# Kernel tuning notes

Measured on AMD Instinct MI355X. Metric: run time of the kernel, lower is better.

The kernel has to match this reference:

```python
import jax, jax.numpy as jnp
import numpy as np

DISTANCE_THRESHOLD = 100.0  # squared-distance threshold (cdist**2 <= thresh)
NO_CODE_ID = -1


def setup_inputs() -> dict:
    key = jax.random.key(0)
    kx, kc = jax.random.split(key)
    x = jax.random.normal(kx, (2, 1024, 64), dtype=jnp.float32)      # [b, s, d] query tokens
    codes = jax.random.normal(kc, (50000, 64), dtype=jnp.float32)    # [n, d] active code bank
    return {"x": x, "codes": codes}


def reference(x, codes):
    # squared euclidean distances, matching torch.cdist(x, codes) ** 2
    x2 = jnp.sum(x * x, axis=-1, keepdims=True)            # [b, s, 1]
    c2 = jnp.sum(codes * codes, axis=-1)                   # [n]
    cross = jnp.einsum('bsd,nd->bsn', x, codes)            # [b, s, n]
    d2 = jnp.maximum(x2 + c2 - 2.0 * cross, 0.0)           # clamp tiny negatives, cdist >= 0

    within = jnp.any(d2 <= DISTANCE_THRESHOLD, axis=-1)    # [b, s]
    nn_ids = jnp.argmin(d2, axis=-1)                       # [b, s]
    return jnp.where(within, nn_ids, NO_CODE_ID)
```

## Files before the change

### kernel.cpp

```cpp
#include <hip/hip_runtime.h>

#define NTOK   2048
#define DIM    64
#define NCODES 50000
#define THRESH 100.0f
#define BIG    3.0e38f
#define MARGIN 4.0f
#define NBLK   391
#define BM32   1564
#define BM32P  1568
#define NCG    64

typedef __attribute__((ext_vector_type(8)))  __bf16 bf16x8;
typedef __attribute__((ext_vector_type(16))) float  float16;

__device__ __forceinline__ unsigned short f2bf(float f) {
    union { float f; unsigned int u; } v; v.f = f;
    unsigned int r = v.u + 0x7FFF + ((v.u >> 16) & 1);
    return (unsigned short)(r >> 16);
}
__device__ __forceinline__ unsigned int pack2(float a, float b) {
    return (unsigned int)f2bf(a) | ((unsigned int)f2bf(b) << 16);
}

__global__ __launch_bounds__(256)
void nn_prep_kernel(const float* __restrict__ x, const float* __restrict__ codes,
                    unsigned short* __restrict__ cbf, unsigned short* __restrict__ xbf,
                    float* __restrict__ c2, float* __restrict__ x2,
                    float* __restrict__ bm32) {
    int g = blockIdx.x * 256 + threadIdx.x;
    if (g < NTOK * 4) {
        int t = g >> 2;
        bm32[(size_t)t * BM32P + BM32 + (g & 3)] = BIG;
    }
    int row = g >> 2;
    int seg = g & 3;
    const float* src;
    unsigned short* dst;
    float* nrm;
    if (row < NCODES) {
        src = codes + (size_t)row * DIM + seg * 16;
        dst = cbf + (size_t)row * DIM + seg * 16;
        nrm = (seg == 0) ? (c2 + row) : nullptr;
    } else if (row < NCODES + NTOK) {
        int r = row - NCODES;
        src = x + (size_t)r * DIM + seg * 16;
        dst = xbf + (size_t)r * DIM + seg * 16;
        nrm = (seg == 0) ? (x2 + r) : nullptr;
    } else {
        return;
    }
    float4 v0 = ((const float4*)src)[0];
    float4 v1 = ((const float4*)src)[1];
    float4 v2 = ((const float4*)src)[2];
    float4 v3 = ((const float4*)src)[3];
    float s = 0.f;
    s = fmaf(v0.x, v0.x, s); s = fmaf(v0.y, v0.y, s);
    s = fmaf(v0.z, v0.z, s); s = fmaf(v0.w, v0.w, s);
    s = fmaf(v1.x, v1.x, s); s = fmaf(v1.y, v1.y, s);
    s = fmaf(v1.z, v1.z, s); s = fmaf(v1.w, v1.w, s);
    s = fmaf(v2.x, v2.x, s); s = fmaf(v2.y, v2.y, s);
    s = fmaf(v2.z, v2.z, s); s = fmaf(v2.w, v2.w, s);
    s = fmaf(v3.x, v3.x, s); s = fmaf(v3.y, v3.y, s);
    s = fmaf(v3.z, v3.z, s); s = fmaf(v3.w, v3.w, s);
    uint4 lo, hi;
    lo.x = pack2(v0.x, v0.y); lo.y = pack2(v0.z, v0.w);
    lo.z = pack2(v1.x, v1.y); lo.w = pack2(v1.z, v1.w);
    hi.x = pack2(v2.x, v2.y); hi.y = pack2(v2.z, v2.w);
    hi.z = pack2(v3.x, v3.y); hi.w = pack2(v3.z, v3.w);
    *(uint4*)dst = lo;
    *(uint4*)(dst + 8) = hi;
    s += __shfl_xor(s, 1);
    s += __shfl_xor(s, 2);
    if (nrm) *nrm = s;
}

__global__ __launch_bounds__(256, 2)
void nn_stageA_kernel(const unsigned short* __restrict__ xbf,
                      const unsigned short* __restrict__ cbf,
                      const float* __restrict__ c2g,
                      float* __restrict__ bm32) {
    __shared__ __bf16 cs[128 * 72];
    __shared__ float  c2s[128];

    const int tid  = threadIdx.x;
    const int w    = tid >> 6;
    const int lane = tid & 63;
    const int l31  = lane & 31;
    const int h    = lane >> 5;
    const int gi   = blockIdx.x;
    const int g0   = 6 * gi + min(gi, 7);
    const int nb   = (gi < 7) ? 7 : 6;
    const int t0   = blockIdx.y * 256;

    bf16x8 bfr[4][2];
#pragma unroll
    for (int s = 0; s < 4; ++s)
#pragma unroll
        for (int nj = 0; nj < 2; ++nj)
            bfr[s][nj] = *(const bf16x8*)&xbf[
                (size_t)(t0 + w * 64 + nj * 32 + l31) * DIM + s * 16 + h * 8];

    uint4 pr[4];
    float prc;
    auto prefetch = [&](int blk) {
        int n0 = blk * 128;
#pragma unroll
        for (int it = 0; it < 4; ++it) {
            int g = it * 256 + tid;
            int row = g >> 3, seg = g & 7;
            int n = n0 + row;
            pr[it] = (n < NCODES) ? *(const uint4*)(cbf + (size_t)n * DIM + seg * 8)
                                  : make_uint4(0, 0, 0, 0);
        }
        if (tid < 128) {
            int n = n0 + tid;
            prc = (n < NCODES) ? c2g[n] : BIG;
        }
    };
    prefetch(g0);

    for (int t = 0; t < nb; ++t) {
        const int blk = g0 + t;
        __syncthreads();

#pragma unroll
        for (int it = 0; it < 4; ++it) {
            int g = it * 256 + tid;
            int row = g >> 3, seg = g & 7;
            *(uint4*)&cs[row * 72 + seg * 8] = pr[it];
        }
        if (tid < 128) c2s[tid] = prc;
        if (t + 1 < nb) prefetch(blk + 1);
        __syncthreads();

        float16 acc[4][2];
#pragma unroll
        for (int mi = 0; mi < 4; ++mi) {
#pragma unroll
            for (int g2 = 0; g2 < 4; ++g2) {
                float4 c4 = *(float4*)&c2s[mi * 32 + g2 * 8 + 4 * h];
#pragma unroll
                for (int i = 0; i < 4; ++i) {
                    float iv = -0.5f * ((float*)&c4)[i];
                    acc[mi][0][g2 * 4 + i] = iv;
                    acc[mi][1][g2 * 4 + i] = iv;
                }
            }
        }

#pragma unroll
        for (int s = 0; s < 4; ++s) {
            bf16x8 a[4];
#pragma unroll
            for (int mi = 0; mi < 4; ++mi)
                a[mi] = *(bf16x8*)&cs[(mi * 32 + l31) * 72 + s * 16 + h * 8];
#pragma unroll
            for (int mi = 0; mi < 4; ++mi)
#pragma unroll
                for (int nj = 0; nj < 2; ++nj)
                    acc[mi][nj] = __builtin_amdgcn_mfma_f32_32x32x16_bf16(
                        a[mi], bfr[s][nj], acc[mi][nj], 0, 0, 0);
        }

#pragma unroll
        for (int nj = 0; nj < 2; ++nj) {
            float4 o;
#pragma unroll
            for (int mi = 0; mi < 4; ++mi) {
                float m = acc[mi][nj][0];
#pragma unroll
                for (int r = 1; r < 16; ++r) m = fmaxf(m, acc[mi][nj][r]);
                m = fmaxf(m, __shfl_xor(m, 32));
                ((float*)&o)[mi] = -2.0f * m;
            }
            if (lane < 32) {
                int token = t0 + w * 64 + nj * 32 + lane;
                *(float4*)&bm32[(size_t)token * BM32P + blk * 4] = o;
            }
        }
    }
}

__global__ __launch_bounds__(256)
void nn_finalize_kernel(const float* __restrict__ x,
                        const float* __restrict__ codes,
                        const float* __restrict__ c2,
                        const float* __restrict__ x2,
                        const float* __restrict__ bm32,
                        int* __restrict__ out) {
    __shared__ float redf[8];
    __shared__ int   redi[4];
    __shared__ int   queue[BM32P];
    __shared__ int   qcount;
    __shared__ float gshare;

    const int tid  = threadIdx.x;
    const int w    = tid >> 6;
    const int lane = tid & 63;
    const int t    = blockIdx.x;
    const float* bm = bm32 + (size_t)t * BM32P;

    if (tid == 0) qcount = 0;

    float v[7];
    float g = BIG;
#pragma unroll
    for (int k = 0; k < 7; ++k) {
        int b = tid + k * 256;
        v[k] = (b < BM32P) ? bm[b] : BIG;
        g = fminf(g, v[k]);
    }
#pragma unroll
    for (int m = 1; m < 64; m <<= 1) g = fminf(g, __shfl_xor(g, m));
    if (lane == 0) redf[w] = g;
    __syncthreads();
    if (tid == 0)
        gshare = fminf(fminf(redf[0], redf[1]), fminf(redf[2], redf[3])) + MARGIN;
    __syncthreads();
    const float th = gshare;

#pragma unroll
    for (int k = 0; k < 7; ++k) {
        int b = tid + k * 256;
        if (b < BM32P && v[k] <= th) {
            int slot = atomicAdd(&qcount, 1);
            queue[slot] = b;
        }
    }
    __syncthreads();
    const int nq = qcount;

    const int half = lane & 1;
    float4 xh[8];
#pragma unroll
    for (int q = 0; q < 8; ++q)
        xh[q] = *(const float4*)(x + (size_t)t * DIM + half * 32 + q * 4);
    const float x2v = x2[t];

    float bv = BIG;
    int   bi = 0x7fffffff;
    for (int e = w; e < nq; e += 4) {
        int blk = queue[e];
        int n = blk * 32 + (lane >> 1);
        if (n < NCODES) {
            const float4* cp = (const float4*)(codes + (size_t)n * DIM + half * 32);
            float d = 0.f;
#pragma unroll
            for (int q = 0; q < 8; ++q) {
                float4 c4 = cp[q];
                d = fmaf(xh[q].x, c4.x, d);
                d = fmaf(xh[q].y, c4.y, d);
                d = fmaf(xh[q].z, c4.z, d);
                d = fmaf(xh[q].w, c4.w, d);
            }
            d += __shfl_xor(d, 1);
            float d2 = fmaxf(fmaf(-2.f, d, x2v + c2[n]), 0.f);
            if (d2 < bv || (d2 == bv && n < bi)) { bv = d2; bi = n; }
        }
    }
#pragma unroll
    for (int m = 1; m < 64; m <<= 1) {
        float vv = __shfl_xor(bv, m);
        int   ii = __shfl_xor(bi, m);
        if (vv < bv || (vv == bv && ii < bi)) { bv = vv; bi = ii; }
    }
    if (lane == 0) { redf[4 + w] = bv; redi[w] = bi; }
    __syncthreads();
    if (tid == 0) {
        float fb = BIG;
        int   fi = 0x7fffffff;
#pragma unroll
        for (int i = 0; i < 4; ++i) {
            float vv = redf[4 + i];
            int   ii = redi[i];
            if (vv < fb || (vv == fb && ii < fi)) { fb = vv; fi = ii; }
        }
        out[t] = (fb <= THRESH) ? fi : -1;
    }
}

extern "C" void kernel_launch(void* const* d_in, const int* in_sizes, int n_in,
                              void* d_out, int out_size, void* d_ws, size_t ws_size,
                              hipStream_t stream) {
    const float* x     = (const float*)d_in[0];
    const float* codes = (const float*)d_in[1];

    float* c2 = (float*)d_ws;
    float* x2 = c2 + 50048;
    unsigned short* cbf = (unsigned short*)(x2 + NTOK);
    unsigned short* xbf = cbf + (size_t)NCODES * DIM;
    float* bm32 = (float*)(xbf + (size_t)NTOK * DIM);
    int* out = (int*)d_out;

    nn_prep_kernel<<<814, 256, 0, stream>>>(x, codes, cbf, xbf, c2, x2, bm32);
    nn_stageA_kernel<<<dim3(NCG, 8), 256, 0, stream>>>(xbf, cbf, c2, bm32);
    nn_finalize_kernel<<<NTOK, 256, 0, stream>>>(x, codes, c2, x2, bm32, out);
}
```

Measured before the change: 107.9 us.

## Fuse bf16 conversion and norm computation into stage A, drop prep kernel

```diff
diff --git a/kernel.cpp b/kernel.cpp
--- a/kernel.cpp
+++ b/kernel.cpp
@@ -22,63 +22,18 @@
 __device__ __forceinline__ unsigned int pack2(float a, float b) {
     return (unsigned int)f2bf(a) | ((unsigned int)f2bf(b) << 16);
 }
-
-__global__ __launch_bounds__(256)
-void nn_prep_kernel(const float* __restrict__ x, const float* __restrict__ codes,
-                    unsigned short* __restrict__ cbf, unsigned short* __restrict__ xbf,
-                    float* __restrict__ c2, float* __restrict__ x2,
-                    float* __restrict__ bm32) {
-    int g = blockIdx.x * 256 + threadIdx.x;
-    if (g < NTOK * 4) {
-        int t = g >> 2;
-        bm32[(size_t)t * BM32P + BM32 + (g & 3)] = BIG;
-    }
-    int row = g >> 2;
-    int seg = g & 3;
-    const float* src;
-    unsigned short* dst;
-    float* nrm;
-    if (row < NCODES) {
-        src = codes + (size_t)row * DIM + seg * 16;
-        dst = cbf + (size_t)row * DIM + seg * 16;
-        nrm = (seg == 0) ? (c2 + row) : nullptr;
-    } else if (row < NCODES + NTOK) {
-        int r = row - NCODES;
-        src = x + (size_t)r * DIM + seg * 16;
-        dst = xbf + (size_t)r * DIM + seg * 16;
-        nrm = (seg == 0) ? (x2 + r) : nullptr;
-    } else {
-        return;
-    }
-    float4 v0 = ((const float4*)src)[0];
-    float4 v1 = ((const float4*)src)[1];
-    float4 v2 = ((const float4*)src)[2];
-    float4 v3 = ((const float4*)src)[3];
-    float s = 0.f;
-    s = fmaf(v0.x, v0.x, s); s = fmaf(v0.y, v0.y, s);
-    s = fmaf(v0.z, v0.z, s); s = fmaf(v0.w, v0.w, s);
-    s = fmaf(v1.x, v1.x, s); s = fmaf(v1.y, v1.y, s);
-    s = fmaf(v1.z, v1.z, s); s = fmaf(v1.w, v1.w, s);
-    s = fmaf(v2.x, v2.x, s); s = fmaf(v2.y, v2.y, s);
-    s = fmaf(v2.z, v2.z, s); s = fmaf(v2.w, v2.w, s);
-    s = fmaf(v3.x, v3.x, s); s = fmaf(v3.y, v3.y, s);
-    s = fmaf(v3.z, v3.z, s); s = fmaf(v3.w, v3.w, s);
-    uint4 lo, hi;
-    lo.x = pack2(v0.x, v0.y); lo.y = pack2(v0.z, v0.w);
-    lo.z = pack2(v1.x, v1.y); lo.w = pack2(v1.z, v1.w);
-    hi.x = pack2(v2.x, v2.y); hi.y = pack2(v2.z, v2.w);
-    hi.z = pack2(v3.x, v3.y); hi.w = pack2(v3.z, v3.w);
-    *(uint4*)dst = lo;
-    *(uint4*)(dst + 8) = hi;
-    s += __shfl_xor(s, 1);
-    s += __shfl_xor(s, 2);
-    if (nrm) *nrm = s;
+__device__ __forceinline__ float max16(const float16& v) {
+    float a = fmaxf(v[0], v[1]),   b = fmaxf(v[2], v[3]);
+    float c = fmaxf(v[4], v[5]),   d = fmaxf(v[6], v[7]);
+    float e = fmaxf(v[8], v[9]),   f = fmaxf(v[10], v[11]);
+    float g = fmaxf(v[12], v[13]), h = fmaxf(v[14], v[15]);
+    a = fmaxf(a, b); c = fmaxf(c, d); e = fmaxf(e, f); g = fmaxf(g, h);
+    return fmaxf(fmaxf(a, c), fmaxf(e, g));
 }
 
 __global__ __launch_bounds__(256, 2)
-void nn_stageA_kernel(const unsigned short* __restrict__ xbf,
-                      const unsigned short* __restrict__ cbf,
-                      const float* __restrict__ c2g,
+void nn_stageA_kernel(const float* __restrict__ x,
+                      const float* __restrict__ codes,
                       float* __restrict__ bm32) {
     __shared__ __bf16 cs[128 * 72];
     __shared__ float  c2s[128];
@@ -92,30 +47,36 @@
     const int g0   = 6 * gi + min(gi, 7);
     const int nb   = (gi < 7) ? 7 : 6;
     const int t0   = blockIdx.y * 256;
+    const int row_ = tid >> 3;
+    const int seg  = tid & 7;
 
     bf16x8 bfr[4][2];
 #pragma unroll
     for (int s = 0; s < 4; ++s)
 #pragma unroll
-        for (int nj = 0; nj < 2; ++nj)
-            bfr[s][nj] = *(const bf16x8*)&xbf[
-                (size_t)(t0 + w * 64 + nj * 32 + l31) * DIM + s * 16 + h * 8];
-
-    uint4 pr[4];
-    float prc;
+        for (int nj = 0; nj < 2; ++nj) {
+            const float4* xp = (const float4*)(x +
+                (size_t)(t0 + w * 64 + nj * 32 + l31) * DIM + s * 16 + h * 8);
+            float4 a = xp[0], b = xp[1];
+            uint4 u;
+            u.x = pack2(a.x, a.y); u.y = pack2(a.z, a.w);
+            u.z = pack2(b.x, b.y); u.w = pack2(b.z, b.w);
+            bfr[s][nj] = *(bf16x8*)&u;
+        }
+
+    float4 pra[4], prb[4];
     auto prefetch = [&](int blk) {
         int n0 = blk * 128;
 #pragma unroll
         for (int it = 0; it < 4; ++it) {
-            int g = it * 256 + tid;
-            int row = g >> 3, seg = g & 7;
-            int n = n0 + row;
-            pr[it] = (n < NCODES) ? *(const uint4*)(cbf + (size_t)n * DIM + seg * 8)
-                                  : make_uint4(0, 0, 0, 0);
-        }
-        if (tid < 128) {
-            int n = n0 + tid;
-            prc = (n < NCODES) ? c2g[n] : BIG;
+            int n = n0 + it * 32 + row_;
+            if (n < NCODES) {
+                const float4* cp = (const float4*)(codes + (size_t)n * DIM + seg * 8);
+                pra[it] = cp[0]; prb[it] = cp[1];
+            } else {
+                pra[it] = make_float4(0.f, 0.f, 0.f, 0.f);
+                prb[it] = pra[it];
+            }
         }
     };
     prefetch(g0);
@@ -126,28 +87,38 @@
 
 #pragma unroll
         for (int it = 0; it < 4; ++it) {
-            int g = it * 256 + tid;
-            int row = g >> 3, seg = g & 7;
-            *(uint4*)&cs[row * 72 + seg * 8] = pr[it];
-        }
-        if (tid < 128) c2s[tid] = prc;
+            int row = it * 32 + row_;
+            float4 a = pra[it], b = prb[it];
+            float s = a.x * a.x;
+            s = fmaf(a.y, a.y, s); s = fmaf(a.z, a.z, s); s = fmaf(a.w, a.w, s);
+            s = fmaf(b.x, b.x, s); s = fmaf(b.y, b.y, s);
+            s = fmaf(b.z, b.z, s); s = fmaf(b.w, b.w, s);
+            s += __shfl_xor(s, 1);
+            s += __shfl_xor(s, 2);
+            s += __shfl_xor(s, 4);
+            uint4 u;
+            u.x = pack2(a.x, a.y); u.y = pack2(a.z, a.w);
+            u.z = pack2(b.x, b.y); u.w = pack2(b.z, b.w);
+            *(uint4*)&cs[row * 72 + seg * 8] = u;
+            if (seg == 0)
+                c2s[row] = (blk * 128 + row < NCODES) ? -0.5f * s : -0.5f * BIG;
+        }
         if (t + 1 < nb) prefetch(blk + 1);
         __syncthreads();
 
         float16 acc[4][2];
 #pragma unroll
-        for (int mi = 0; mi < 4; ++mi) {
+        for (int mi = 0; mi < 4; ++mi)
 #pragma unroll
             for (int g2 = 0; g2 < 4; ++g2) {
                 float4 c4 = *(float4*)&c2s[mi * 32 + g2 * 8 + 4 * h];
 #pragma unroll
                 for (int i = 0; i < 4; ++i) {
-                    float iv = -0.5f * ((float*)&c4)[i];
+                    float iv = ((float*)&c4)[i];
                     acc[mi][0][g2 * 4 + i] = iv;
                     acc[mi][1][g2 * 4 + i] = iv;
                 }
             }
-        }
 
 #pragma unroll
         for (int s = 0; s < 4; ++s) {
@@ -163,35 +134,29 @@
                         a[mi], bfr[s][nj], acc[mi][nj], 0, 0, 0);
         }
 
-#pragma unroll
-        for (int nj = 0; nj < 2; ++nj) {
-            float4 o;
+        float4 o[2];
+#pragma unroll
+        for (int nj = 0; nj < 2; ++nj)
 #pragma unroll
             for (int mi = 0; mi < 4; ++mi) {
-                float m = acc[mi][nj][0];
-#pragma unroll
-                for (int r = 1; r < 16; ++r) m = fmaxf(m, acc[mi][nj][r]);
+                float m = max16(acc[mi][nj]);
                 m = fmaxf(m, __shfl_xor(m, 32));
-                ((float*)&o)[mi] = -2.0f * m;
-            }
-            if (lane < 32) {
-                int token = t0 + w * 64 + nj * 32 + lane;
-                *(float4*)&bm32[(size_t)token * BM32P + blk * 4] = o;
-            }
-        }
+                ((float*)&o[nj])[mi] = -2.0f * m;
+            }
+        float4 ov = (lane < 32) ? o[0] : o[1];
+        int token = t0 + w * 64 + lane;
+        *(float4*)&bm32[(size_t)token * BM32P + blk * 4] = ov;
     }
 }
 
 __global__ __launch_bounds__(256)
 void nn_finalize_kernel(const float* __restrict__ x,
                         const float* __restrict__ codes,
-                        const float* __restrict__ c2,
-                        const float* __restrict__ x2,
                         const float* __restrict__ bm32,
                         int* __restrict__ out) {
     __shared__ float redf[8];
     __shared__ int   redi[4];
-    __shared__ int   queue[BM32P];
+    __shared__ int   queue[BM32];
     __shared__ int   qcount;
     __shared__ float gshare;
 
@@ -208,7 +173,7 @@
 #pragma unroll
     for (int k = 0; k < 7; ++k) {
         int b = tid + k * 256;
-        v[k] = (b < BM32P) ? bm[b] : BIG;
+        v[k] = (b < BM32) ? bm[b] : BIG;
         g = fminf(g, v[k]);
     }
 #pragma unroll
@@ -223,7 +188,7 @@
 #pragma unroll
     for (int k = 0; k < 7; ++k) {
         int b = tid + k * 256;
-        if (b < BM32P && v[k] <= th) {
+        if (v[k] <= th) {
             int slot = atomicAdd(&qcount, 1);
             queue[slot] = b;
         }
@@ -236,7 +201,15 @@
 #pragma unroll
     for (int q = 0; q < 8; ++q)
         xh[q] = *(const float4*)(x + (size_t)t * DIM + half * 32 + q * 4);
-    const float x2v = x2[t];
+    float x2v = 0.f;
+#pragma unroll
+    for (int q = 0; q < 8; ++q) {
+        x2v = fmaf(xh[q].x, xh[q].x, x2v);
+        x2v = fmaf(xh[q].y, xh[q].y, x2v);
+        x2v = fmaf(xh[q].z, xh[q].z, x2v);
+        x2v = fmaf(xh[q].w, xh[q].w, x2v);
+    }
+    x2v += __shfl_xor(x2v, 1);
 
     float bv = BIG;
     int   bi = 0x7fffffff;
@@ -245,17 +218,22 @@
         int n = blk * 32 + (lane >> 1);
         if (n < NCODES) {
             const float4* cp = (const float4*)(codes + (size_t)n * DIM + half * 32);
-            float d = 0.f;
+            float d = 0.f, cq = 0.f;
 #pragma unroll
             for (int q = 0; q < 8; ++q) {
                 float4 c4 = cp[q];
-                d = fmaf(xh[q].x, c4.x, d);
-                d = fmaf(xh[q].y, c4.y, d);
-                d = fmaf(xh[q].z, c4.z, d);
-                d = fmaf(xh[q].w, c4.w, d);
-            }
-            d += __shfl_xor(d, 1);
-            float d2 = fmaxf(fmaf(-2.f, d, x2v + c2[n]), 0.f);
+                d  = fmaf(xh[q].x, c4.x, d);
+                d  = fmaf(xh[q].y, c4.y, d);
+                d  = fmaf(xh[q].z, c4.z, d);
+                d  = fmaf(xh[q].w, c4.w, d);
+                cq = fmaf(c4.x, c4.x, cq);
+                cq = fmaf(c4.y, c4.y, cq);
+                cq = fmaf(c4.z, c4.z, cq);
+                cq = fmaf(c4.w, c4.w, cq);
+            }
+            d  += __shfl_xor(d, 1);
+            cq += __shfl_xor(cq, 1);
+            float d2 = fmaxf(fmaf(-2.f, d, x2v + cq), 0.f);
             if (d2 < bv || (d2 == bv && n < bi)) { bv = d2; bi = n; }
         }
     }
@@ -285,15 +263,9 @@
                               hipStream_t stream) {
     const float* x     = (const float*)d_in[0];
     const float* codes = (const float*)d_in[1];
-
-    float* c2 = (float*)d_ws;
-    float* x2 = c2 + 50048;
-    unsigned short* cbf = (unsigned short*)(x2 + NTOK);
-    unsigned short* xbf = cbf + (size_t)NCODES * DIM;
-    float* bm32 = (float*)(xbf + (size_t)NTOK * DIM);
+    float* bm32 = (float*)d_ws;
     int* out = (int*)d_out;
 
-    nn_prep_kernel<<<814, 256, 0, stream>>>(x, codes, cbf, xbf, c2, x2, bm32);
-    nn_stageA_kernel<<<dim3(NCG, 8), 256, 0, stream>>>(xbf, cbf, c2, bm32);
-    nn_finalize_kernel<<<NTOK, 256, 0, stream>>>(x, codes, c2, x2, bm32, out);
-}
+    nn_stageA_kernel<<<dim3(NCG, 8), 256, 0, stream>>>(x, codes, bm32);
+    nn_finalize_kernel<<<NTOK, 256, 0, stream>>>(x, codes, bm32, out);
+}
```

New measurement: 131.3 us. 1.22x slower.

## Coarsen block bounds to 128 codes, double code groups, transpose bound layout

Applied to the files above, without the earlier changes.

```diff
diff --git a/kernel.cpp b/kernel.cpp
--- a/kernel.cpp
+++ b/kernel.cpp
@@ -7,9 +7,7 @@
 #define BIG    3.0e38f
 #define MARGIN 4.0f
 #define NBLK   391
-#define BM32   1564
-#define BM32P  1568
-#define NCG    64
+#define NCG    128
 
 typedef __attribute__((ext_vector_type(8)))  __bf16 bf16x8;
 typedef __attribute__((ext_vector_type(16))) float  float16;
@@ -22,17 +20,20 @@
 __device__ __forceinline__ unsigned int pack2(float a, float b) {
     return (unsigned int)f2bf(a) | ((unsigned int)f2bf(b) << 16);
 }
+__device__ __forceinline__ float max16(const float16& v) {
+    float a = fmaxf(v[0], v[1]),   b = fmaxf(v[2], v[3]);
+    float c = fmaxf(v[4], v[5]),   d = fmaxf(v[6], v[7]);
+    float e = fmaxf(v[8], v[9]),   f = fmaxf(v[10], v[11]);
+    float g = fmaxf(v[12], v[13]), h = fmaxf(v[14], v[15]);
+    a = fmaxf(a, b); c = fmaxf(c, d); e = fmaxf(e, f); g = fmaxf(g, h);
+    return fmaxf(fmaxf(a, c), fmaxf(e, g));
+}
 
 __global__ __launch_bounds__(256)
 void nn_prep_kernel(const float* __restrict__ x, const float* __restrict__ codes,
                     unsigned short* __restrict__ cbf, unsigned short* __restrict__ xbf,
-                    float* __restrict__ c2, float* __restrict__ x2,
-                    float* __restrict__ bm32) {
+                    float* __restrict__ c2) {
     int g = blockIdx.x * 256 + threadIdx.x;
-    if (g < NTOK * 4) {
-        int t = g >> 2;
-        bm32[(size_t)t * BM32P + BM32 + (g & 3)] = BIG;
-    }
     int row = g >> 2;
     int seg = g & 3;
     const float* src;
@@ -46,7 +47,7 @@
         int r = row - NCODES;
         src = x + (size_t)r * DIM + seg * 16;
         dst = xbf + (size_t)r * DIM + seg * 16;
-        nrm = (seg == 0) ? (x2 + r) : nullptr;
+        nrm = nullptr;
     } else {
         return;
     }
@@ -79,7 +80,7 @@
 void nn_stageA_kernel(const unsigned short* __restrict__ xbf,
                       const unsigned short* __restrict__ cbf,
                       const float* __restrict__ c2g,
-                      float* __restrict__ bm32) {
+                      float* __restrict__ bmF) {
     __shared__ __bf16 cs[128 * 72];
     __shared__ float  c2s[128];
 
@@ -89,8 +90,8 @@
     const int l31  = lane & 31;
     const int h    = lane >> 5;
     const int gi   = blockIdx.x;
-    const int g0   = 6 * gi + min(gi, 7);
-    const int nb   = (gi < 7) ? 7 : 6;
+    const int g0   = 3 * gi + min(gi, 7);
+    const int nb   = (gi < 7) ? 4 : 3;
     const int t0   = blockIdx.y * 256;
 
     bf16x8 bfr[4][2];
@@ -130,24 +131,23 @@
             int row = g >> 3, seg = g & 7;
             *(uint4*)&cs[row * 72 + seg * 8] = pr[it];
         }
-        if (tid < 128) c2s[tid] = prc;
+        if (tid < 128) c2s[tid] = -0.5f * prc;
         if (t + 1 < nb) prefetch(blk + 1);
         __syncthreads();
 
         float16 acc[4][2];
 #pragma unroll
-        for (int mi = 0; mi < 4; ++mi) {
+        for (int mi = 0; mi < 4; ++mi)
 #pragma unroll
             for (int g2 = 0; g2 < 4; ++g2) {
                 float4 c4 = *(float4*)&c2s[mi * 32 + g2 * 8 + 4 * h];
 #pragma unroll
                 for (int i = 0; i < 4; ++i) {
-                    float iv = -0.5f * ((float*)&c4)[i];
+                    float iv = ((float*)&c4)[i];
                     acc[mi][0][g2 * 4 + i] = iv;
                     acc[mi][1][g2 * 4 + i] = iv;
                 }
             }
-        }
 
 #pragma unroll
         for (int s = 0; s < 4; ++s) {
@@ -163,54 +163,44 @@
                         a[mi], bfr[s][nj], acc[mi][nj], 0, 0, 0);
         }
 
+        float sv[2];
 #pragma unroll
         for (int nj = 0; nj < 2; ++nj) {
-            float4 o;
-#pragma unroll
-            for (int mi = 0; mi < 4; ++mi) {
-                float m = acc[mi][nj][0];
-#pragma unroll
-                for (int r = 1; r < 16; ++r) m = fmaxf(m, acc[mi][nj][r]);
-                m = fmaxf(m, __shfl_xor(m, 32));
-                ((float*)&o)[mi] = -2.0f * m;
-            }
-            if (lane < 32) {
-                int token = t0 + w * 64 + nj * 32 + lane;
-                *(float4*)&bm32[(size_t)token * BM32P + blk * 4] = o;
-            }
-        }
+            float m = max16(acc[0][nj]);
+            m = fmaxf(m, max16(acc[1][nj]));
+            m = fmaxf(m, max16(acc[2][nj]));
+            m = fmaxf(m, max16(acc[3][nj]));
+            m = fmaxf(m, __shfl_xor(m, 32));
+            sv[nj] = -2.0f * m;
+        }
+        bmF[(size_t)blk * NTOK + t0 + w * 64 + lane] = (lane < 32) ? sv[0] : sv[1];
     }
 }
 
 __global__ __launch_bounds__(256)
 void nn_finalize_kernel(const float* __restrict__ x,
                         const float* __restrict__ codes,
-                        const float* __restrict__ c2,
-                        const float* __restrict__ x2,
-                        const float* __restrict__ bm32,
+                        const float* __restrict__ bmF,
                         int* __restrict__ out) {
     __shared__ float redf[8];
     __shared__ int   redi[4];
-    __shared__ int   queue[BM32P];
+    __shared__ int   queue[NBLK];
     __shared__ int   qcount;
     __shared__ float gshare;
 
     const int tid  = threadIdx.x;
     const int w    = tid >> 6;
     const int lane = tid & 63;
-    const int t    = blockIdx.x;
-    const float* bm = bm32 + (size_t)t * BM32P;
+    const int bid  = blockIdx.x;
+    const int t    = (bid & 7) * 256 + (bid >> 3);
+    const float* bp = bmF + t;
 
     if (tid == 0) qcount = 0;
 
-    float v[7];
-    float g = BIG;
-#pragma unroll
-    for (int k = 0; k < 7; ++k) {
-        int b = tid + k * 256;
-        v[k] = (b < BM32P) ? bm[b] : BIG;
-        g = fminf(g, v[k]);
-    }
+    float v0 = (tid < NBLK) ? bp[(size_t)tid * NTOK] : BIG;
+    float v1 = (tid + 256 < NBLK) ? bp[(size_t)(tid + 256) * NTOK] : BIG;
+
+    float g = fminf(v0, v1);
 #pragma unroll
     for (int m = 1; m < 64; m <<= 1) g = fminf(g, __shfl_xor(g, m));
     if (lane == 0) redf[w] = g;
@@ -220,14 +210,8 @@
     __syncthreads();
     const float th = gshare;
 
-#pragma unroll
-    for (int k = 0; k < 7; ++k) {
-        int b = tid + k * 256;
-        if (b < BM32P && v[k] <= th) {
-            int slot = atomicAdd(&qcount, 1);
-            queue[slot] = b;
-        }
-    }
+    if (v0 <= th) queue[atomicAdd(&qcount, 1)] = tid;
+    if (tid + 256 < NBLK && v1 <= th) queue[atomicAdd(&qcount, 1)] = tid + 256;
     __syncthreads();
     const int nq = qcount;
 
@@ -236,26 +220,39 @@
 #pragma unroll
     for (int q = 0; q < 8; ++q)
         xh[q] = *(const float4*)(x + (size_t)t * DIM + half * 32 + q * 4);
-    const float x2v = x2[t];
+    float x2v = 0.f;
+#pragma unroll
+    for (int q = 0; q < 8; ++q) {
+        x2v = fmaf(xh[q].x, xh[q].x, x2v);
+        x2v = fmaf(xh[q].y, xh[q].y, x2v);
+        x2v = fmaf(xh[q].z, xh[q].z, x2v);
+        x2v = fmaf(xh[q].w, xh[q].w, x2v);
+    }
+    x2v += __shfl_xor(x2v, 1);
 
     float bv = BIG;
     int   bi = 0x7fffffff;
-    for (int e = w; e < nq; e += 4) {
+    for (int e = 0; e < nq; ++e) {
         int blk = queue[e];
-        int n = blk * 32 + (lane >> 1);
+        int n = blk * 128 + w * 32 + (lane >> 1);
         if (n < NCODES) {
             const float4* cp = (const float4*)(codes + (size_t)n * DIM + half * 32);
-            float d = 0.f;
+            float d = 0.f, cq = 0.f;
 #pragma unroll
             for (int q = 0; q < 8; ++q) {
                 float4 c4 = cp[q];
-                d = fmaf(xh[q].x, c4.x, d);
-                d = fmaf(xh[q].y, c4.y, d);
-                d = fmaf(xh[q].z, c4.z, d);
-                d = fmaf(xh[q].w, c4.w, d);
+                d  = fmaf(xh[q].x, c4.x, d);
+                d  = fmaf(xh[q].y, c4.y, d);
+                d  = fmaf(xh[q].z, c4.z, d);
+                d  = fmaf(xh[q].w, c4.w, d);
+                cq = fmaf(c4.x, c4.x, cq);
+                cq = fmaf(c4.y, c4.y, cq);
+                cq = fmaf(c4.z, c4.z, cq);
+                cq = fmaf(c4.w, c4.w, cq);
             }
-            d += __shfl_xor(d, 1);
-            float d2 = fmaxf(fmaf(-2.f, d, x2v + c2[n]), 0.f);
+            d  += __shfl_xor(d, 1);
+            cq += __shfl_xor(cq, 1);
+            float d2 = fmaxf(fmaf(-2.f, d, x2v + cq), 0.f);
             if (d2 < bv || (d2 == bv && n < bi)) { bv = d2; bi = n; }
         }
     }
@@ -287,13 +284,12 @@
     const float* codes = (const float*)d_in[1];
 
     float* c2 = (float*)d_ws;
-    float* x2 = c2 + 50048;
-    unsigned short* cbf = (unsigned short*)(x2 + NTOK);
+    unsigned short* cbf = (unsigned short*)(c2 + 50048);
     unsigned short* xbf = cbf + (size_t)NCODES * DIM;
-    float* bm32 = (float*)(xbf + (size_t)NTOK * DIM);
+    float* bmF = (float*)(xbf + (size_t)NTOK * DIM);
     int* out = (int*)d_out;
 
-    nn_prep_kernel<<<814, 256, 0, stream>>>(x, codes, cbf, xbf, c2, x2, bm32);
-    nn_stageA_kernel<<<dim3(NCG, 8), 256, 0, stream>>>(xbf, cbf, c2, bm32);
-    nn_finalize_kernel<<<NTOK, 256, 0, stream>>>(x, codes, c2, x2, bm32, out);
-}
+    nn_prep_kernel<<<814, 256, 0, stream>>>(x, codes, cbf, xbf, c2);
+    nn_stageA_kernel<<<dim3(NCG, 8), 256, 0, stream>>>(xbf, cbf, c2, bmF);
+    nn_finalize_kernel<<<NTOK, 256, 0, stream>>>(x, codes, bmF, out);
+}
```

Measured after the change: 151.6 us. +40.5%, slower.
